# Optimization experiments

Measured on AMD Instinct MI355X. Metric: run time of the kernel, lower is better.

The kernel has to match this reference:

```python
import jax, jax.numpy as jnp
import numpy as np

B, C, H, W = 16, 256, 64, 64
HEADS = 8


def setup_inputs() -> dict:
    key = jax.random.key(0)
    ks = jax.random.split(key, 12)
    s = 0.02
    return {
        "x": jax.random.normal(ks[0], (B, C, H, W), jnp.float32),
        "Wq": jax.random.normal(ks[1], (C, C), jnp.float32) * s,
        "bq": jnp.zeros((C,), jnp.float32),
        "Wk": jax.random.normal(ks[2], (C, C), jnp.float32) * s,
        "bk": jnp.zeros((C,), jnp.float32),
        "Wv": jax.random.normal(ks[3], (C, C), jnp.float32) * s,
        "bv": jnp.zeros((C,), jnp.float32),
        "gamma": jax.random.normal(ks[4], (1,), jnp.float32) * 0.5,
        "beta": jax.random.normal(ks[5], (1,), jnp.float32) * 0.5,
        "W1": jax.random.normal(ks[6], (C, C), jnp.float32) * s,
        "b1": jnp.zeros((C,), jnp.float32),
        "u1": jax.random.normal(ks[7], (C,), jnp.float32),
        "W2": jax.random.normal(ks[8], (C, C), jnp.float32) * s,
        "b2": jnp.zeros((C,), jnp.float32),
        "u2": jax.random.normal(ks[9], (C,), jnp.float32),
    }


def _conv1x1(x, Wt, b):
    # 1x1 conv == per-pixel GEMM over channels
    return jnp.einsum('oc,bchw->bohw', Wt, x) + b[None, :, None, None]


def _l2(v):
    return v / (jnp.linalg.norm(v) + 1e-12)


def _spectral_norm(Wt, u):
    # one power iteration (torch SpectralNorm wrapper), u treated as buffer
    Wm = Wt.reshape(Wt.shape[0], -1)
    v = _l2(Wm.T @ u)
    u_new = _l2(Wm @ v)
    sigma = u_new @ (Wm @ v)
    return Wt / sigma


def reference(x, Wq, bq, Wk, bk, Wv, bv, gamma, beta, W1, b1, u1, W2, b2, u2):
    Bn, Cn, Hh, Ww = x.shape
    N = Hh * Ww
    d = Cn // HEADS
    scale = HEADS ** (-0.5)
    # 1x1 conv projections, then b (h n) s layout -> (B, heads, d, N)
    q = _conv1x1(x, Wq, bq).reshape(Bn, HEADS, d, N)
    k = _conv1x1(x, Wk, bk).reshape(Bn, HEADS, d, N)
    v = _conv1x1(x, Wv, bv).reshape(Bn, HEADS, d, N)
    # per-head channel attention: energy is (B, heads, d, d)
    energy = jnp.einsum('bhis,bhjs->bhij', q, k) * scale
    attn = jax.nn.softmax(energy, axis=-1)
    out = jnp.einsum('bhij,bhjs->bhis', attn, v).reshape(Bn, Cn, Hh, Ww)
    out = gamma * out + x
    # residual refinement net (dropout = identity in eval mode)
    y = _conv1x1(out, _spectral_norm(W1, u1), b1)
    y = jax.nn.leaky_relu(y, 0.1)
    y = _conv1x1(y, _spectral_norm(W2, u2), b2)
    out = out + beta * y
    return (out, attn)
```

## Files before the change

kernel.cpp:

```cpp
#include <hip/hip_runtime.h>
#include <hip/hip_bf16.h>
#include <cstdint>
#include <cstddef>

typedef __attribute__((ext_vector_type(8))) __bf16 bf16x8;
typedef __attribute__((ext_vector_type(4))) float f32x4;
typedef __attribute__((ext_vector_type(8))) unsigned short us8;
typedef __attribute__((ext_vector_type(4))) unsigned short us4;

__device__ __forceinline__ unsigned short f2bf(float f){
  unsigned int u = __float_as_uint(f);
  u += 0x7fffu + ((u >> 16) & 1u);
  return (unsigned short)(u >> 16);
}
__device__ __forceinline__ float bf2f(unsigned short h){
  return __uint_as_float(((unsigned int)h) << 16);
}
__device__ __forceinline__ bf16x8 ldbf8(const unsigned short* p){
  return __builtin_bit_cast(bf16x8, *(const us8*)p);
}

#define SCALE_E 0.35355339059327373f

static const size_t OFF_XHI    = 0;
static const size_t OFF_XLO    = 33554432;
static const size_t OFF_XTHI   = 67108864;
static const size_t OFF_GPART  = 100663296;
static const size_t OFF_G      = 113246208;
static const size_t OFF_M      = 117440512;
static const size_t OFF_W1S    = 119537664;
static const size_t OFF_W2S    = 119668736;
static const size_t OFF_SIG    = 119799808;
static const size_t OFF_XSUM   = 119799824;
static const size_t OFF_ROWADD = 119816208;

__global__ void k_zero(float* __restrict__ xsum){
  xsum[blockIdx.x * 256 + threadIdx.x] = 0.f;
}

__global__ void k_sigma(const float* __restrict__ W1, const float* __restrict__ u1,
                        const float* __restrict__ W2, const float* __restrict__ u2,
                        float* __restrict__ sig){
  const float* W = blockIdx.x ? W2 : W1;
  const float* u = blockIdx.x ? u2 : u1;
  int t = threadIdx.x;
  __shared__ __align__(16) float red[256];
  __shared__ __align__(16) float vls[256];
  __shared__ __align__(16) float uls[256];
  uls[t] = u[t];
  __syncthreads();
  float t1 = 0.f;
  for (int o = 0; o < 256; ++o) t1 += W[o*256 + t] * uls[o];
  red[t] = t1 * t1;
  __syncthreads();
  for (int s = 128; s > 0; s >>= 1){ if (t < s) red[t] += red[t+s]; __syncthreads(); }
  float nrm = sqrtf(red[0]);
  vls[t] = t1 / (nrm + 1e-12f);
  __syncthreads();
  float w = 0.f;
  const float4* wr4 = (const float4*)(W + t*256);
  for (int c4 = 0; c4 < 64; ++c4){
    float4 a = wr4[c4];
    float4 v = *(const float4*)&vls[c4*4];
    w += a.x*v.x + a.y*v.y + a.z*v.z + a.w*v.w;
  }
  __syncthreads();
  red[t] = w * w;
  __syncthreads();
  for (int s = 128; s > 0; s >>= 1){ if (t < s) red[t] += red[t+s]; __syncthreads(); }
  if (t == 0){
    float s2 = red[0];
    float sn = sqrtf(s2);
    sig[blockIdx.x] = s2 / (sn + 1e-12f);
  }
}

__global__ void k_wconv(const float* __restrict__ W1, const float* __restrict__ W2,
                        const float* __restrict__ sig,
                        unsigned short* __restrict__ W1s, unsigned short* __restrict__ W2s){
  int sel = blockIdx.x >> 6;
  const float* W = sel ? W2 : W1;
  unsigned short* o = sel ? W2s : W1s;
  float inv = 1.0f / sig[sel];
  int base = (blockIdx.x & 63) * 1024 + threadIdx.x * 4;
  float4 v = *(const float4*)&W[base];
  us4 r = { f2bf(v.x*inv), f2bf(v.y*inv), f2bf(v.z*inv), f2bf(v.w*inv) };
  *(us4*)&o[base] = r;
}

__global__ __launch_bounds__(256) void k_convert(const float* __restrict__ x,
    unsigned short* __restrict__ xhi, unsigned short* __restrict__ xlo,
    unsigned short* __restrict__ xthi, float* __restrict__ xsum){
  int b = blockIdx.z, c0 = blockIdx.y*64, n0 = blockIdx.x*64;
  int t = threadIdx.x, tn = t & 15, tc = t >> 4;
  __shared__ __align__(16) unsigned short hs[64][68];
  __shared__ __align__(16) float ps[64][17];
  #pragma unroll
  for (int rr = 0; rr < 4; ++rr){
    int cl = rr*16 + tc;
    size_t gro = ((size_t)(b*256 + c0 + cl))*4096 + n0 + tn*4;
    float4 v = *(const float4*)&x[gro];
    unsigned short h0=f2bf(v.x), h1=f2bf(v.y), h2=f2bf(v.z), h3=f2bf(v.w);
    us4 hv = {h0,h1,h2,h3};
    us4 lv = { f2bf(v.x - bf2f(h0)), f2bf(v.y - bf2f(h1)),
               f2bf(v.z - bf2f(h2)), f2bf(v.w - bf2f(h3)) };
    *(us4*)&xhi[gro] = hv;
    *(us4*)&xlo[gro] = lv;
    *(us4*)&hs[cl][tn*4] = hv;
    ps[cl][tn] = v.x + v.y + v.z + v.w;
  }
  __syncthreads();
  #pragma unroll
  for (int rr = 0; rr < 4; ++rr){
    int nl = rr*16 + tc;
    int cl4 = tn*4;
    us4 w = { hs[cl4+0][nl], hs[cl4+1][nl], hs[cl4+2][nl], hs[cl4+3][nl] };
    *(us4*)&xthi[((size_t)(b*4096 + n0 + nl))*256 + c0 + cl4] = w;
  }
  if (t < 64){
    float s = 0.f;
    #pragma unroll
    for (int k = 0; k < 16; ++k) s += ps[t][k];
    atomicAdd(&xsum[b*256 + c0 + t], s);
  }
}

__global__ __launch_bounds__(256) void k_gram(const unsigned short* __restrict__ xhi,
    const unsigned short* __restrict__ xlo, float* __restrict__ G, float* __restrict__ Gp){
  int b = blockIdx.z;
  int tr = (blockIdx.y >> 1) * 128, tc = (blockIdx.y & 1) * 128;
  int kc = blockIdx.x * 1024;
  int t = threadIdx.x;
  __shared__ __align__(16) unsigned short Ah[128*40], Al[128*40], Bh[128*40], Bl[128*40];
  f32x4 acc[4][4];
  #pragma unroll
  for (int i = 0; i < 4; ++i)
    #pragma unroll
    for (int j = 0; j < 4; ++j) acc[i][j] = (f32x4){0.f,0.f,0.f,0.f};
  int srow = t >> 1, skh = (t & 1) * 16;
  int l = t & 63, wv = t >> 6;
  int wr = (wv >> 1) * 64, wc = (wv & 1) * 64;
  int lr = l & 15, lg = l >> 4;
  size_t bb = (size_t)b * 256 * 4096;
  for (int kk = kc; kk < kc + 1024; kk += 32){
    __syncthreads();
    size_t ga = bb + (size_t)(tr + srow)*4096 + kk + skh;
    size_t gb = bb + (size_t)(tc + srow)*4096 + kk + skh;
    *(us8*)&Ah[srow*40 + skh]     = *(const us8*)&xhi[ga];
    *(us8*)&Ah[srow*40 + skh + 8] = *(const us8*)&xhi[ga + 8];
    *(us8*)&Al[srow*40 + skh]     = *(const us8*)&xlo[ga];
    *(us8*)&Al[srow*40 + skh + 8] = *(const us8*)&xlo[ga + 8];
    *(us8*)&Bh[srow*40 + skh]     = *(const us8*)&xhi[gb];
    *(us8*)&Bh[srow*40 + skh + 8] = *(const us8*)&xhi[gb + 8];
    *(us8*)&Bl[srow*40 + skh]     = *(const us8*)&xlo[gb];
    *(us8*)&Bl[srow*40 + skh + 8] = *(const us8*)&xlo[gb + 8];
    __syncthreads();
    bf16x8 ah[4], alv[4], bh[4], blv[4];
    #pragma unroll
    for (int i = 0; i < 4; ++i){
      ah[i]  = ldbf8(&Ah[(wr + i*16 + lr)*40 + lg*8]);
      alv[i] = ldbf8(&Al[(wr + i*16 + lr)*40 + lg*8]);
      bh[i]  = ldbf8(&Bh[(wc + i*16 + lr)*40 + lg*8]);
      blv[i] = ldbf8(&Bl[(wc + i*16 + lr)*40 + lg*8]);
    }
    #pragma unroll
    for (int i = 0; i < 4; ++i)
      #pragma unroll
      for (int j = 0; j < 4; ++j){
        acc[i][j] = __builtin_amdgcn_mfma_f32_16x16x32_bf16(ah[i],  bh[j],  acc[i][j], 0,0,0);
        acc[i][j] = __builtin_amdgcn_mfma_f32_16x16x32_bf16(ah[i],  blv[j], acc[i][j], 0,0,0);
        acc[i][j] = __builtin_amdgcn_mfma_f32_16x16x32_bf16(alv[i], bh[j],  acc[i][j], 0,0,0);
      }
  }
  float* dst = (blockIdx.x == 0) ? (G + (size_t)b*65536)
                                 : (Gp + ((size_t)(blockIdx.x - 1)*16 + b)*65536);
  #pragma unroll
  for (int i = 0; i < 4; ++i)
    #pragma unroll
    for (int j = 0; j < 4; ++j)
      #pragma unroll
      for (int r = 0; r < 4; ++r){
        int row = tr + wr + i*16 + lg*4 + r;
        int col = tc + wc + j*16 + lr;
        dst[row*256 + col] = acc[i][j][r];
      }
}

__global__ void k_gred(float* __restrict__ G, const float* __restrict__ Gp){
  size_t idx = ((size_t)blockIdx.x * 256 + threadIdx.x) * 4;
  float4 g  = *(float4*)&G[idx];
  float4 p0 = *(const float4*)&Gp[idx];
  float4 p1 = *(const float4*)&Gp[idx + 1048576];
  float4 p2 = *(const float4*)&Gp[idx + 2097152];
  g.x += p0.x + p1.x + p2.x;  g.y += p0.y + p1.y + p2.y;
  g.z += p0.z + p1.z + p2.z;  g.w += p0.w + p1.w + p2.w;
  *(float4*)&G[idx] = g;
}

__global__ __launch_bounds__(256) void k_attn(const float* __restrict__ G,
    const float* __restrict__ Wq, const float* __restrict__ bq,
    const float* __restrict__ Wk, const float* __restrict__ bk,
    const float* __restrict__ Wv, const float* __restrict__ bv,
    const float* __restrict__ gptr, const float* __restrict__ xsum,
    unsigned short* __restrict__ Mw, float* __restrict__ rowadd,
    float* __restrict__ attn_out){
  int bh = blockIdx.x, b = bh >> 3, h = bh & 7;
  int t = threadIdx.x;
  __shared__ __align__(16) float Qh[32*256];
  __shared__ __align__(16) float Tl[32*260];
  __shared__ __align__(16) float El[32*36];
  __shared__ __align__(16) float Aw[32*36];
  __shared__ float qsv[32], ksv[32];
  {
    const float4* wq4 = (const float4*)(Wq + (size_t)h*32*256);
    float4* qh4 = (float4*)Qh;
    #pragma unroll
    for (int it = 0; it < 8; ++it) qh4[it*256 + t] = wq4[it*256 + t];
  }
  __syncthreads();
  float Tr[32];
  #pragma unroll
  for (int i = 0; i < 32; ++i) Tr[i] = 0.f;
  const float* Grow = G + ((size_t)b*256 + t)*256;
  for (int c4 = 0; c4 < 64; ++c4){
    float4 g4 = *(const float4*)&Grow[c4*4];
    #pragma unroll
    for (int i = 0; i < 32; ++i){
      float4 q4 = *(const float4*)&Qh[i*256 + c4*4];
      Tr[i] += q4.x*g4.x + q4.y*g4.y + q4.z*g4.z + q4.w*g4.w;
    }
  }
  #pragma unroll
  for (int i = 0; i < 32; ++i) Tl[i*260 + t] = Tr[i];
  if (t < 32){
    float s = 0.f; const float* qr = Qh + t*256; const float* xs = xsum + b*256;
    for (int c = 0; c < 256; ++c) s += qr[c]*xs[c];
    qsv[t] = s;
  } else if (t < 64){
    int j = t - 32; float s = 0.f;
    const float* kr = Wk + (size_t)(h*32 + j)*256; const float* xs = xsum + b*256;
    for (int c = 0; c < 256; ++c) s += kr[c]*xs[c];
    ksv[j] = s;
  }
  __syncthreads();
  {
    int i = t >> 3, jb = (t & 7) * 4;
    float e0=0.f, e1=0.f, e2=0.f, e3=0.f;
    const float* Ti = Tl + i*260;
    const float* k0 = Wk + (size_t)(h*32 + jb + 0)*256;
    const float* k1 = Wk + (size_t)(h*32 + jb + 1)*256;
    const float* k2 = Wk + (size_t)(h*32 + jb + 2)*256;
    const float* k3 = Wk + (size_t)(h*32 + jb + 3)*256;
    for (int c4 = 0; c4 < 64; ++c4){
      float4 tv = *(const float4*)&Ti[c4*4];
      float4 a0 = *(const float4*)&k0[c4*4];
      float4 a1 = *(const float4*)&k1[c4*4];
      float4 a2 = *(const float4*)&k2[c4*4];
      float4 a3 = *(const float4*)&k3[c4*4];
      e0 += tv.x*a0.x + tv.y*a0.y + tv.z*a0.z + tv.w*a0.w;
      e1 += tv.x*a1.x + tv.y*a1.y + tv.z*a1.z + tv.w*a1.w;
      e2 += tv.x*a2.x + tv.y*a2.y + tv.z*a2.z + tv.w*a2.w;
      e3 += tv.x*a3.x + tv.y*a3.y + tv.z*a3.z + tv.w*a3.w;
    }
    float bqi = bq[h*32 + i];
    float e[4] = {e0,e1,e2,e3};
    #pragma unroll
    for (int jj = 0; jj < 4; ++jj){
      float bkj = bk[h*32 + jb + jj];
      El[i*36 + jb + jj] = SCALE_E * (e[jj] + bqi*ksv[jb+jj] + bkj*qsv[i] + 4096.f*bqi*bkj);
    }
  }
  __syncthreads();
  if (t < 32){
    float m = -1e30f;
    #pragma unroll
    for (int j = 0; j < 32; ++j) m = fmaxf(m, El[t*36 + j]);
    float ex[32]; float s = 0.f;
    #pragma unroll
    for (int j = 0; j < 32; ++j){ ex[j] = expf(El[t*36 + j] - m); s += ex[j]; }
    float inv = 1.f / s;
    float* ao = attn_out + (((size_t)(b*8 + h))*32 + t)*32;
    #pragma unroll
    for (int j = 0; j < 32; ++j){ float a = ex[j]*inv; Aw[t*36 + j] = a; ao[j] = a; }
  }
  __syncthreads();
  float gamma = gptr[0];
  float mr[32];
  #pragma unroll
  for (int i = 0; i < 32; ++i) mr[i] = 0.f;
  for (int j = 0; j < 32; ++j){
    float wvv = Wv[(size_t)(h*32 + j)*256 + t];
    #pragma unroll
    for (int i = 0; i < 32; ++i) mr[i] += Aw[i*36 + j] * wvv;
  }
  unsigned short* Mrow = Mw + ((size_t)b*256 + h*32)*256 + t;
  #pragma unroll
  for (int i = 0; i < 32; ++i) Mrow[i*256] = f2bf(gamma * mr[i]);
  if (t < 32){
    float s = 0.f;
    #pragma unroll
    for (int j = 0; j < 32; ++j) s += Aw[t*36 + j] * bv[h*32 + j];
    rowadd[b*256 + h*32 + t] = gamma * s;
  }
}

template<int MODE>
__global__ __launch_bounds__(256) void k_gemm(const unsigned short* __restrict__ Aall,
    const unsigned short* __restrict__ Bmat, const unsigned short* __restrict__ xthi,
    const float* __restrict__ rowadd, const float* __restrict__ bias,
    const float* __restrict__ betap, float* __restrict__ osc,
    unsigned short* __restrict__ outb){
  int b = blockIdx.z;
  int n0 = blockIdx.x * 128, o0 = blockIdx.y * 128;
  int t = threadIdx.x;
  __shared__ __align__(16) unsigned short Als[128*40], Bls[128*40];
  f32x4 acc[4][4];
  #pragma unroll
  for (int i = 0; i < 4; ++i)
    #pragma unroll
    for (int j = 0; j < 4; ++j) acc[i][j] = (f32x4){0.f,0.f,0.f,0.f};
  const unsigned short* A  = Aall + (size_t)b * 1048576;
  const unsigned short* Bp = (MODE == 0) ? (Bmat + (size_t)b * 65536) : Bmat;
  int srow = t >> 1, skh = (t & 1) * 16;
  int l = t & 63, wv = t >> 6;
  int wr = (wv >> 1) * 64, wc = (wv & 1) * 64;
  int lr = l & 15, lg = l >> 4;
  for (int kk = 0; kk < 256; kk += 32){
    __syncthreads();
    const unsigned short* ga = A  + (size_t)(n0 + srow)*256 + kk + skh;
    const unsigned short* gb = Bp + (size_t)(o0 + srow)*256 + kk + skh;
    *(us8*)&Als[srow*40 + skh]     = *(const us8*)ga;
    *(us8*)&Als[srow*40 + skh + 8] = *(const us8*)(ga + 8);
    *(us8*)&Bls[srow*40 + skh]     = *(const us8*)gb;
    *(us8*)&Bls[srow*40 + skh + 8] = *(const us8*)(gb + 8);
    __syncthreads();
    bf16x8 af[4], bfv[4];
    #pragma unroll
    for (int i = 0; i < 4; ++i) af[i]  = ldbf8(&Als[(wr + i*16 + lr)*40 + lg*8]);
    #pragma unroll
    for (int j = 0; j < 4; ++j) bfv[j] = ldbf8(&Bls[(wc + j*16 + lr)*40 + lg*8]);
    #pragma unroll
    for (int i = 0; i < 4; ++i)
      #pragma unroll
      for (int j = 0; j < 4; ++j)
        acc[i][j] = __builtin_amdgcn_mfma_f32_16x16x32_bf16(af[i], bfv[j], acc[i][j], 0,0,0);
  }
  float beta = (MODE == 2) ? betap[0] : 0.f;
  #pragma unroll
  for (int j = 0; j < 4; ++j){
    int oc = o0 + wc + j*16 + lr;
    float bvl = (MODE == 0) ? rowadd[b*256 + oc] : bias[oc];
    #pragma unroll
    for (int i = 0; i < 4; ++i){
      #pragma unroll
      for (int r = 0; r < 4; ++r){
        int n = n0 + wr + i*16 + lg*4 + r;
        size_t off = ((size_t)b*4096 + n)*256 + oc;
        float v = acc[i][j][r];
        if (MODE == 0){
          v += bf2f(xthi[off]) + bvl;
          osc[off] = v;
          outb[off] = f2bf(v);
        } else if (MODE == 1){
          v += bvl;
          v = (v > 0.f) ? v : 0.1f * v;
          outb[off] = f2bf(v);
        } else {
          v = osc[off] + beta * (v + bvl);
          outb[off] = f2bf(v);
        }
      }
    }
  }
}

__global__ __launch_bounds__(256) void k_tpose(const unsigned short* __restrict__ fin,
                                               float* __restrict__ out){
  int b = blockIdx.z, c0 = blockIdx.y*64, n0 = blockIdx.x*64;
  int t = threadIdx.x, tn = t & 15, tc = t >> 4;
  __shared__ __align__(16) unsigned short ts[64][68];
  #pragma unroll
  for (int rr = 0; rr < 4; ++rr){
    int nl = rr*16 + tc;
    us4 v = *(const us4*)&fin[((size_t)(b*4096 + n0 + nl))*256 + c0 + tn*4];
    *(us4*)&ts[nl][tn*4] = v;
  }
  __syncthreads();
  #pragma unroll
  for (int rr = 0; rr < 4; ++rr){
    int cl = rr*16 + tc;
    int nl4 = tn*4;
    float4 v = { bf2f(ts[nl4+0][cl]), bf2f(ts[nl4+1][cl]),
                 bf2f(ts[nl4+2][cl]), bf2f(ts[nl4+3][cl]) };
    *(float4*)&out[((size_t)(b*256 + c0 + cl))*4096 + n0 + nl4] = v;
  }
}

extern "C" void kernel_launch(void* const* d_in, const int* in_sizes, int n_in,
                              void* d_out, int out_size, void* d_ws, size_t ws_size,
                              hipStream_t stream){
  const float* x    = (const float*)d_in[0];
  const float* Wq   = (const float*)d_in[1];
  const float* bq   = (const float*)d_in[2];
  const float* Wk   = (const float*)d_in[3];
  const float* bk   = (const float*)d_in[4];
  const float* Wv   = (const float*)d_in[5];
  const float* bv   = (const float*)d_in[6];
  const float* gamma= (const float*)d_in[7];
  const float* beta = (const float*)d_in[8];
  const float* W1   = (const float*)d_in[9];
  const float* b1   = (const float*)d_in[10];
  const float* u1   = (const float*)d_in[11];
  const float* W2   = (const float*)d_in[12];
  const float* b2   = (const float*)d_in[13];
  const float* u2   = (const float*)d_in[14];

  char* ws = (char*)d_ws;
  unsigned short* xhi   = (unsigned short*)(ws + OFF_XHI);
  unsigned short* xlo   = (unsigned short*)(ws + OFF_XLO);
  unsigned short* xthi  = (unsigned short*)(ws + OFF_XTHI);
  float*          Gp    = (float*)(ws + OFF_GPART);
  float*          G     = (float*)(ws + OFF_G);
  unsigned short* Mw    = (unsigned short*)(ws + OFF_M);
  unsigned short* W1s   = (unsigned short*)(ws + OFF_W1S);
  unsigned short* W2s   = (unsigned short*)(ws + OFF_W2S);
  float*          sig   = (float*)(ws + OFF_SIG);
  float*          xsum  = (float*)(ws + OFF_XSUM);
  float*          rowadd= (float*)(ws + OFF_ROWADD);
  unsigned short* othi  = xlo;
  unsigned short* y1t   = xhi;
  unsigned short* finT  = xthi;

  float* outF  = (float*)d_out;
  float* attnO = outF + 16777216;
  float* osc   = outF;

  k_zero<<<dim3(16), dim3(256), 0, stream>>>(xsum);
  k_sigma<<<dim3(2), dim3(256), 0, stream>>>(W1, u1, W2, u2, sig);
  k_wconv<<<dim3(128), dim3(256), 0, stream>>>(W1, W2, sig, W1s, W2s);
  k_convert<<<dim3(64,4,16), dim3(256), 0, stream>>>(x, xhi, xlo, xthi, xsum);
  k_gram<<<dim3(4,4,16), dim3(256), 0, stream>>>(xhi, xlo, G, Gp);
  k_gred<<<dim3(1024), dim3(256), 0, stream>>>(G, Gp);
  k_attn<<<dim3(128), dim3(256), 0, stream>>>(G, Wq, bq, Wk, bk, Wv, bv,
                                              gamma, xsum, Mw, rowadd, attnO);
  k_gemm<0><<<dim3(32,2,16), dim3(256), 0, stream>>>(xthi, Mw, xthi, rowadd, b1, beta, osc, othi);
  k_gemm<1><<<dim3(32,2,16), dim3(256), 0, stream>>>(othi, W1s, xthi, rowadd, b1, beta, osc, y1t);
  k_gemm<2><<<dim3(32,2,16), dim3(256), 0, stream>>>(y1t, W2s, xthi, rowadd, b2, beta, osc, finT);
  k_tpose<<<dim3(64,4,16), dim3(256), 0, stream>>>(finT, outF);
}
```

Baseline: 446.4 us.

## Compute attention energy via split-bf16 MFMA GEMMs instead of scalar FP32 loops

The single per-head k_attn kernel, which computed T = Wq_h·G and E = T·Wk_h^T with scalar FP32 loops, is replaced by two batched MFMA GEMM kernels, k_qg and k_e. They compute Wq·G and then (Wq·G)·Wk^T over full 256×256 matrices, using a hi/lo bf16 split that keeps near-FP32 accuracy. k_gred now emits G as hi/lo bf16, and a slimmer k_soft does the bias corrections and a shuffle-based softmax. The full product also computes the off-diagonal head blocks, which wastes about 8x the needed FLOPs and adds intermediate buffers and launches, in exchange for running on the matrix cores.

```diff
diff --git a/kernel.cpp b/kernel.cpp
--- a/kernel.cpp
+++ b/kernel.cpp
@@ -18,6 +18,20 @@
 }
 __device__ __forceinline__ bf16x8 ldbf8(const unsigned short* p){
   return __builtin_bit_cast(bf16x8, *(const us8*)p);
+}
+__device__ __forceinline__ void split16(const float* __restrict__ g,
+                                        unsigned short* __restrict__ hs,
+                                        unsigned short* __restrict__ ls){
+  #pragma unroll
+  for (int q = 0; q < 4; ++q){
+    float4 v = *(const float4*)(g + q*4);
+    unsigned short h0=f2bf(v.x), h1=f2bf(v.y), h2=f2bf(v.z), h3=f2bf(v.w);
+    us4 hv = {h0,h1,h2,h3};
+    us4 lv = { f2bf(v.x - bf2f(h0)), f2bf(v.y - bf2f(h1)),
+               f2bf(v.z - bf2f(h2)), f2bf(v.w - bf2f(h3)) };
+    *(us4*)(hs + q*4) = hv;
+    *(us4*)(ls + q*4) = lv;
+  }
 }
 
 #define SCALE_E 0.35355339059327373f
@@ -186,121 +200,199 @@
       }
 }
 
-__global__ void k_gred(float* __restrict__ G, const float* __restrict__ Gp){
+__global__ void k_gred(const float* __restrict__ G0, const float* __restrict__ Gp,
+                       unsigned short* __restrict__ Ghi, unsigned short* __restrict__ Glo){
   size_t idx = ((size_t)blockIdx.x * 256 + threadIdx.x) * 4;
-  float4 g  = *(float4*)&G[idx];
+  float4 g  = *(const float4*)&G0[idx];
   float4 p0 = *(const float4*)&Gp[idx];
   float4 p1 = *(const float4*)&Gp[idx + 1048576];
   float4 p2 = *(const float4*)&Gp[idx + 2097152];
-  g.x += p0.x + p1.x + p2.x;  g.y += p0.y + p1.y + p2.y;
-  g.z += p0.z + p1.z + p2.z;  g.w += p0.w + p1.w + p2.w;
-  *(float4*)&G[idx] = g;
-}
-
-__global__ __launch_bounds__(256) void k_attn(const float* __restrict__ G,
+  float s0 = g.x + p0.x + p1.x + p2.x;
+  float s1 = g.y + p0.y + p1.y + p2.y;
+  float s2 = g.z + p0.z + p1.z + p2.z;
+  float s3 = g.w + p0.w + p1.w + p2.w;
+  unsigned short h0=f2bf(s0), h1=f2bf(s1), h2=f2bf(s2), h3=f2bf(s3);
+  us4 hv = {h0,h1,h2,h3};
+  us4 lv = { f2bf(s0 - bf2f(h0)), f2bf(s1 - bf2f(h1)),
+             f2bf(s2 - bf2f(h2)), f2bf(s3 - bf2f(h3)) };
+  *(us4*)&Ghi[idx] = hv;
+  *(us4*)&Glo[idx] = lv;
+}
+
+__global__ __launch_bounds__(256) void k_qg(const float* __restrict__ Wq,
+    const unsigned short* __restrict__ Ghi, const unsigned short* __restrict__ Glo,
+    unsigned short* __restrict__ Phi, unsigned short* __restrict__ Plo){
+  int b = blockIdx.z;
+  int tr = blockIdx.y * 128, tc = blockIdx.x * 128;
+  int t = threadIdx.x;
+  __shared__ __align__(16) unsigned short Ah[128*40], Al[128*40], Bh[128*40], Bl[128*40];
+  f32x4 acc[4][4];
+  #pragma unroll
+  for (int i = 0; i < 4; ++i)
+    #pragma unroll
+    for (int j = 0; j < 4; ++j) acc[i][j] = (f32x4){0.f,0.f,0.f,0.f};
+  int srow = t >> 1, skh = (t & 1) * 16;
+  int l = t & 63, wv = t >> 6;
+  int wr = (wv >> 1) * 64, wc = (wv & 1) * 64;
+  int lr = l & 15, lg = l >> 4;
+  for (int kk = 0; kk < 256; kk += 32){
+    __syncthreads();
+    split16(Wq + (size_t)(tr + srow)*256 + kk + skh, &Ah[srow*40 + skh], &Al[srow*40 + skh]);
+    size_t gb = (size_t)b*65536 + (size_t)(tc + srow)*256 + kk + skh;
+    *(us8*)&Bh[srow*40 + skh]     = *(const us8*)&Ghi[gb];
+    *(us8*)&Bh[srow*40 + skh + 8] = *(const us8*)&Ghi[gb + 8];
+    *(us8*)&Bl[srow*40 + skh]     = *(const us8*)&Glo[gb];
+    *(us8*)&Bl[srow*40 + skh + 8] = *(const us8*)&Glo[gb + 8];
+    __syncthreads();
+    bf16x8 ah[4], alv[4], bh[4], blv[4];
+    #pragma unroll
+    for (int i = 0; i < 4; ++i){
+      ah[i]  = ldbf8(&Ah[(wr + i*16 + lr)*40 + lg*8]);
+      alv[i] = ldbf8(&Al[(wr + i*16 + lr)*40 + lg*8]);
+      bh[i]  = ldbf8(&Bh[(wc + i*16 + lr)*40 + lg*8]);
+      blv[i] = ldbf8(&Bl[(wc + i*16 + lr)*40 + lg*8]);
+    }
+    #pragma unroll
+    for (int i = 0; i < 4; ++i)
+      #pragma unroll
+      for (int j = 0; j < 4; ++j){
+        acc[i][j] = __builtin_amdgcn_mfma_f32_16x16x32_bf16(ah[i],  bh[j],  acc[i][j], 0,0,0);
+        acc[i][j] = __builtin_amdgcn_mfma_f32_16x16x32_bf16(ah[i],  blv[j], acc[i][j], 0,0,0);
+        acc[i][j] = __builtin_amdgcn_mfma_f32_16x16x32_bf16(alv[i], bh[j],  acc[i][j], 0,0,0);
+      }
+  }
+  #pragma unroll
+  for (int i = 0; i < 4; ++i)
+    #pragma unroll
+    for (int j = 0; j < 4; ++j)
+      #pragma unroll
+      for (int r = 0; r < 4; ++r){
+        int row = tr + wr + i*16 + lg*4 + r;
+        int col = tc + wc + j*16 + lr;
+        size_t off = (size_t)b*65536 + (size_t)row*256 + col;
+        float p = acc[i][j][r];
+        unsigned short hp = f2bf(p);
+        Phi[off] = hp;
+        Plo[off] = f2bf(p - bf2f(hp));
+      }
+}
+
+__global__ __launch_bounds__(256) void k_e(const unsigned short* __restrict__ Phi,
+    const unsigned short* __restrict__ Plo, const float* __restrict__ Wk,
+    float* __restrict__ Ef){
+  int b = blockIdx.z;
+  int tr = blockIdx.y * 128, tc = blockIdx.x * 128;
+  int t = threadIdx.x;
+  __shared__ __align__(16) unsigned short Ah[128*40], Al[128*40], Bh[128*40], Bl[128*40];
+  f32x4 acc[4][4];
+  #pragma unroll
+  for (int i = 0; i < 4; ++i)
+    #pragma unroll
+    for (int j = 0; j < 4; ++j) acc[i][j] = (f32x4){0.f,0.f,0.f,0.f};
+  int srow = t >> 1, skh = (t & 1) * 16;
+  int l = t & 63, wv = t >> 6;
+  int wr = (wv >> 1) * 64, wc = (wv & 1) * 64;
+  int lr = l & 15, lg = l >> 4;
+  for (int kk = 0; kk < 256; kk += 32){
+    __syncthreads();
+    size_t ga = (size_t)b*65536 + (size_t)(tr + srow)*256 + kk + skh;
+    *(us8*)&Ah[srow*40 + skh]     = *(const us8*)&Phi[ga];
+    *(us8*)&Ah[srow*40 + skh + 8] = *(const us8*)&Phi[ga + 8];
+    *(us8*)&Al[srow*40 + skh]     = *(const us8*)&Plo[ga];
+    *(us8*)&Al[srow*40 + skh + 8] = *(const us8*)&Plo[ga + 8];
+    split16(Wk + (size_t)(tc + srow)*256 + kk + skh, &Bh[srow*40 + skh], &Bl[srow*40 + skh]);
+    __syncthreads();
+    bf16x8 ah[4], alv[4], bh[4], blv[4];
+    #pragma unroll
+    for (int i = 0; i < 4; ++i){
+      ah[i]  = ldbf8(&Ah[(wr + i*16 + lr)*40 + lg*8]);
+      alv[i] = ldbf8(&Al[(wr + i*16 + lr)*40 + lg*8]);
+      bh[i]  = ldbf8(&Bh[(wc + i*16 + lr)*40 + lg*8]);
+      blv[i] = ldbf8(&Bl[(wc + i*16 + lr)*40 + lg*8]);
+    }
+    #pragma unroll
+    for (int i = 0; i < 4; ++i)
+      #pragma unroll
+      for (int j = 0; j < 4; ++j){
+        acc[i][j] = __builtin_amdgcn_mfma_f32_16x16x32_bf16(ah[i],  bh[j],  acc[i][j], 0,0,0);
+        acc[i][j] = __builtin_amdgcn_mfma_f32_16x16x32_bf16(ah[i],  blv[j], acc[i][j], 0,0,0);
+        acc[i][j] = __builtin_amdgcn_mfma_f32_16x16x32_bf16(alv[i], bh[j],  acc[i][j], 0,0,0);
+      }
+  }
+  #pragma unroll
+  for (int i = 0; i < 4; ++i)
+    #pragma unroll
+    for (int j = 0; j < 4; ++j)
+      #pragma unroll
+      for (int r = 0; r < 4; ++r){
+        int row = tr + wr + i*16 + lg*4 + r;
+        int col = tc + wc + j*16 + lr;
+        Ef[(size_t)b*65536 + (size_t)row*256 + col] = SCALE_E * acc[i][j][r];
+      }
+}
+
+__global__ __launch_bounds__(256) void k_soft(const float* __restrict__ Ef,
     const float* __restrict__ Wq, const float* __restrict__ bq,
     const float* __restrict__ Wk, const float* __restrict__ bk,
     const float* __restrict__ Wv, const float* __restrict__ bv,
     const float* __restrict__ gptr, const float* __restrict__ xsum,
     unsigned short* __restrict__ Mw, float* __restrict__ rowadd,
     float* __restrict__ attn_out){
-  int bh = blockIdx.x, b = bh >> 3, h = bh & 7;
+  int blk = blockIdx.x, b = blk >> 3, h = blk & 7;
   int t = threadIdx.x;
-  __shared__ __align__(16) float Qh[32*256];
-  __shared__ __align__(16) float Tl[32*260];
-  __shared__ __align__(16) float El[32*36];
-  __shared__ __align__(16) float Aw[32*36];
+  int i = t >> 3, j4 = (t & 7) * 4;
+  __shared__ __align__(16) float Aw[32][40];
   __shared__ float qsv[32], ksv[32];
-  {
-    const float4* wq4 = (const float4*)(Wq + (size_t)h*32*256);
-    float4* qh4 = (float4*)Qh;
-    #pragma unroll
-    for (int it = 0; it < 8; ++it) qh4[it*256 + t] = wq4[it*256 + t];
-  }
-  __syncthreads();
-  float Tr[32];
-  #pragma unroll
-  for (int i = 0; i < 32; ++i) Tr[i] = 0.f;
-  const float* Grow = G + ((size_t)b*256 + t)*256;
-  for (int c4 = 0; c4 < 64; ++c4){
-    float4 g4 = *(const float4*)&Grow[c4*4];
-    #pragma unroll
-    for (int i = 0; i < 32; ++i){
-      float4 q4 = *(const float4*)&Qh[i*256 + c4*4];
-      Tr[i] += q4.x*g4.x + q4.y*g4.y + q4.z*g4.z + q4.w*g4.w;
+  if (t < 64){
+    int r = t & 31;
+    const float* Wm = (t < 32) ? Wq : Wk;
+    const float4* wr4 = (const float4*)(Wm + (size_t)(h*32 + r)*256);
+    const float4* xs4 = (const float4*)(xsum + b*256);
+    float s = 0.f;
+    #pragma unroll
+    for (int c4 = 0; c4 < 64; ++c4){
+      float4 a = wr4[c4], xv = xs4[c4];
+      s += a.x*xv.x + a.y*xv.y + a.z*xv.z + a.w*xv.w;
     }
-  }
-  #pragma unroll
-  for (int i = 0; i < 32; ++i) Tl[i*260 + t] = Tr[i];
-  if (t < 32){
-    float s = 0.f; const float* qr = Qh + t*256; const float* xs = xsum + b*256;
-    for (int c = 0; c < 256; ++c) s += qr[c]*xs[c];
-    qsv[t] = s;
-  } else if (t < 64){
-    int j = t - 32; float s = 0.f;
-    const float* kr = Wk + (size_t)(h*32 + j)*256; const float* xs = xsum + b*256;
-    for (int c = 0; c < 256; ++c) s += kr[c]*xs[c];
-    ksv[j] = s;
-  }
-  __syncthreads();
-  {
-    int i = t >> 3, jb = (t & 7) * 4;
-    float e0=0.f, e1=0.f, e2=0.f, e3=0.f;
-    const float* Ti = Tl + i*260;
-    const float* k0 = Wk + (size_t)(h*32 + jb + 0)*256;
-    const float* k1 = Wk + (size_t)(h*32 + jb + 1)*256;
-    const float* k2 = Wk + (size_t)(h*32 + jb + 2)*256;
-    const float* k3 = Wk + (size_t)(h*32 + jb + 3)*256;
-    for (int c4 = 0; c4 < 64; ++c4){
-      float4 tv = *(const float4*)&Ti[c4*4];
-      float4 a0 = *(const float4*)&k0[c4*4];
-      float4 a1 = *(const float4*)&k1[c4*4];
-      float4 a2 = *(const float4*)&k2[c4*4];
-      float4 a3 = *(const float4*)&k3[c4*4];
-      e0 += tv.x*a0.x + tv.y*a0.y + tv.z*a0.z + tv.w*a0.w;
-      e1 += tv.x*a1.x + tv.y*a1.y + tv.z*a1.z + tv.w*a1.w;
-      e2 += tv.x*a2.x + tv.y*a2.y + tv.z*a2.z + tv.w*a2.w;
-      e3 += tv.x*a3.x + tv.y*a3.y + tv.z*a3.z + tv.w*a3.w;
-    }
-    float bqi = bq[h*32 + i];
-    float e[4] = {e0,e1,e2,e3};
-    #pragma unroll
-    for (int jj = 0; jj < 4; ++jj){
-      float bkj = bk[h*32 + jb + jj];
-      El[i*36 + jb + jj] = SCALE_E * (e[jj] + bqi*ksv[jb+jj] + bkj*qsv[i] + 4096.f*bqi*bkj);
-    }
-  }
-  __syncthreads();
-  if (t < 32){
-    float m = -1e30f;
-    #pragma unroll
-    for (int j = 0; j < 32; ++j) m = fmaxf(m, El[t*36 + j]);
-    float ex[32]; float s = 0.f;
-    #pragma unroll
-    for (int j = 0; j < 32; ++j){ ex[j] = expf(El[t*36 + j] - m); s += ex[j]; }
-    float inv = 1.f / s;
-    float* ao = attn_out + (((size_t)(b*8 + h))*32 + t)*32;
-    #pragma unroll
-    for (int j = 0; j < 32; ++j){ float a = ex[j]*inv; Aw[t*36 + j] = a; ao[j] = a; }
-  }
+    if (t < 32) qsv[r] = s; else ksv[r] = s;
+  }
+  __syncthreads();
+  float4 e = *(const float4*)&Ef[(size_t)b*65536 + (size_t)(h*32 + i)*256 + h*32 + j4];
+  float bqi = bq[h*32 + i];
+  float qb  = qsv[i] + 4096.f * bqi;
+  e.x += SCALE_E * (bqi*ksv[j4+0] + bk[h*32+j4+0]*qb);
+  e.y += SCALE_E * (bqi*ksv[j4+1] + bk[h*32+j4+1]*qb);
+  e.z += SCALE_E * (bqi*ksv[j4+2] + bk[h*32+j4+2]*qb);
+  e.w += SCALE_E * (bqi*ksv[j4+3] + bk[h*32+j4+3]*qb);
+  float m = fmaxf(fmaxf(e.x, e.y), fmaxf(e.z, e.w));
+  m = fmaxf(m, __shfl_xor(m, 1));
+  m = fmaxf(m, __shfl_xor(m, 2));
+  m = fmaxf(m, __shfl_xor(m, 4));
+  float ex0 = expf(e.x - m), ex1 = expf(e.y - m), ex2 = expf(e.z - m), ex3 = expf(e.w - m);
+  float s = ex0 + ex1 + ex2 + ex3;
+  s += __shfl_xor(s, 1); s += __shfl_xor(s, 2); s += __shfl_xor(s, 4);
+  float inv = 1.f / s;
+  float4 a4 = { ex0*inv, ex1*inv, ex2*inv, ex3*inv };
+  *(float4*)&attn_out[(((size_t)(b*8 + h))*32 + i)*32 + j4] = a4;
+  *(float4*)&Aw[i][j4] = a4;
   __syncthreads();
   float gamma = gptr[0];
   float mr[32];
   #pragma unroll
-  for (int i = 0; i < 32; ++i) mr[i] = 0.f;
+  for (int r = 0; r < 32; ++r) mr[r] = 0.f;
   for (int j = 0; j < 32; ++j){
     float wvv = Wv[(size_t)(h*32 + j)*256 + t];
     #pragma unroll
-    for (int i = 0; i < 32; ++i) mr[i] += Aw[i*36 + j] * wvv;
+    for (int r = 0; r < 32; ++r) mr[r] += Aw[r][j] * wvv;
   }
   unsigned short* Mrow = Mw + ((size_t)b*256 + h*32)*256 + t;
   #pragma unroll
-  for (int i = 0; i < 32; ++i) Mrow[i*256] = f2bf(gamma * mr[i]);
+  for (int r = 0; r < 32; ++r) Mrow[r*256] = f2bf(gamma * mr[r]);
   if (t < 32){
-    float s = 0.f;
-    #pragma unroll
-    for (int j = 0; j < 32; ++j) s += Aw[t*36 + j] * bv[h*32 + j];
-    rowadd[b*256 + h*32 + t] = gamma * s;
+    float sr = 0.f;
+    #pragma unroll
+    for (int j = 0; j < 32; ++j) sr += Aw[t][j] * bv[h*32 + j];
+    rowadd[b*256 + h*32 + t] = gamma * sr;
   }
 }
 
@@ -420,13 +512,18 @@
   unsigned short* xlo   = (unsigned short*)(ws + OFF_XLO);
   unsigned short* xthi  = (unsigned short*)(ws + OFF_XTHI);
   float*          Gp    = (float*)(ws + OFF_GPART);
-  float*          G     = (float*)(ws + OFF_G);
+  float*          G0    = (float*)(ws + OFF_G);
   unsigned short* Mw    = (unsigned short*)(ws + OFF_M);
   unsigned short* W1s   = (unsigned short*)(ws + OFF_W1S);
   unsigned short* W2s   = (unsigned short*)(ws + OFF_W2S);
   float*          sig   = (float*)(ws + OFF_SIG);
   float*          xsum  = (float*)(ws + OFF_XSUM);
   float*          rowadd= (float*)(ws + OFF_ROWADD);
+  unsigned short* Ghi   = (unsigned short*)(ws + OFF_XLO);
+  unsigned short* Glo   = (unsigned short*)(ws + OFF_XLO + 2097152);
+  unsigned short* Phi   = (unsigned short*)(ws + OFF_GPART);
+  unsigned short* Plo   = (unsigned short*)(ws + OFF_GPART + 2097152);
+  float*          Ef    = (float*)(ws + OFF_GPART + 4194304);
   unsigned short* othi  = xlo;
   unsigned short* y1t   = xhi;
   unsigned short* finT  = xthi;
@@ -439,9 +536,11 @@
   k_sigma<<<dim3(2), dim3(256), 0, stream>>>(W1, u1, W2, u2, sig);
   k_wconv<<<dim3(128), dim3(256), 0, stream>>>(W1, W2, sig, W1s, W2s);
   k_convert<<<dim3(64,4,16), dim3(256), 0, stream>>>(x, xhi, xlo, xthi, xsum);
-  k_gram<<<dim3(4,4,16), dim3(256), 0, stream>>>(xhi, xlo, G, Gp);
-  k_gred<<<dim3(1024), dim3(256), 0, stream>>>(G, Gp);
-  k_attn<<<dim3(128), dim3(256), 0, stream>>>(G, Wq, bq, Wk, bk, Wv, bv,
+  k_gram<<<dim3(4,4,16), dim3(256), 0, stream>>>(xhi, xlo, G0, Gp);
+  k_gred<<<dim3(1024), dim3(256), 0, stream>>>(G0, Gp, Ghi, Glo);
+  k_qg<<<dim3(2,2,16), dim3(256), 0, stream>>>(Wq, Ghi, Glo, Phi, Plo);
+  k_e<<<dim3(2,2,16), dim3(256), 0, stream>>>(Phi, Plo, Wk, Ef);
+  k_soft<<<dim3(128), dim3(256), 0, stream>>>(Ef, Wq, bq, Wk, bk, Wv, bv,
                                               gamma, xsum, Mw, rowadd, attnO);
   k_gemm<0><<<dim3(32,2,16), dim3(256), 0, stream>>>(xthi, Mw, xthi, rowadd, b1, beta, osc, othi);
   k_gemm<1><<<dim3(32,2,16), dim3(256), 0, stream>>>(othi, W1s, xthi, rowadd, b1, beta, osc, y1t);
```

After: 424.5 us. 4.9% less time.
